# Performance work log

Measured on AMD Instinct MI355X. Metric: run time of the kernel, lower is better.

## Reference

```python
import jax, jax.numpy as jnp
import numpy as np

B, S, D = 4, 2048, 128


def setup_inputs() -> dict:
    key = jax.random.key(0)
    kq, kk, kv = jax.random.split(key, 3)
    query = jax.random.normal(kq, (B, S, D), dtype=jnp.float32)
    key_t = jax.random.normal(kk, (B, S, D), dtype=jnp.float32)
    value = jax.random.normal(kv, (B, S, D), dtype=jnp.float32)
    return {"query": query, "key": key_t, "value": value}


def reference(query, key, value):
    # Raw dot-general attention: contract only the last dim, NO batch dims,
    # so scores have shape [B, Sq, B, Sk] (cross-batch attention).
    scores = jnp.einsum('aqd,bkd->aqbk', query, key)  # [B,S,B,S]
    # softmax over the trailing half of the dims (axes 2 and 3 jointly)
    attn = jax.nn.softmax(scores, axis=(2, 3))
    # Dropout: train=False -> deterministic no-op.
    # Second dot_general contracts trailing (B,Sk) of attn with leading (B,Sk) of value.
    y = jnp.einsum('aqbk,bkd->aqd', attn, value)  # [B,S,D]
    return y
```

## Files before the change

### kernel.cpp

```cpp
#include <hip/hip_runtime.h>
#include <hip/hip_bf16.h>
#include <string.h>

#define NROWS 8192
#define DH    128
#define G     8
#define KPG   (NROWS / G)
#define NIT   (KPG / 64)
#define B32U  (16 * 512)
#define LOG2E 1.44269504088896340736f
#define MSCALED (56.0f * LOG2E)

typedef __attribute__((ext_vector_type(8)))  short    short8;
typedef __attribute__((ext_vector_type(16))) float    floatx16;
typedef __attribute__((ext_vector_type(4)))  unsigned short us4;
typedef __attribute__((ext_vector_type(8)))  _Float16 half8;
typedef __attribute__((ext_vector_type(4)))  _Float16 half4;

#define MFMA_BF32(a, b, c)  __builtin_amdgcn_mfma_f32_32x32x16_bf16((a), (b), (c), 0, 0, 0)
#define MFMA_F16W(a, b, c)  __builtin_amdgcn_mfma_f32_32x32x16_f16((a), (b), (c), 0, 0, 0)

__device__ __forceinline__ unsigned short f32_to_bf16(float f) {
    union { float f; unsigned u; } v; v.f = f;
    unsigned u = v.u + 0x7FFFu + ((v.u >> 16) & 1u);
    return (unsigned short)(u >> 16);
}
__device__ __forceinline__ float bf16_to_f32(unsigned short h) {
    union { unsigned u; float f; } v; v.u = ((unsigned)h) << 16;
    return v.f;
}
__device__ __forceinline__ float fast_exp2(float x) {
    float r; asm("v_exp_f32 %0, %1" : "=v"(r) : "v"(x)); return r;
}
__device__ __forceinline__ void async_ld16(const void* g, void* lds) {
    __builtin_amdgcn_global_load_lds(
        (const __attribute__((address_space(1))) unsigned int*)g,
        (__attribute__((address_space(3))) unsigned int*)lds, 16, 0, 0);
}

__global__ void prep_kernel(const float* __restrict__ Q, const float* __restrict__ K,
                            const float* __restrict__ V,
                            _Float16* __restrict__ Qf, unsigned short* __restrict__ KV) {
    int bid = blockIdx.x;
    if (bid < 1024) {
        int i = bid * 1024 + threadIdx.x * 4;
        float4 q = *(const float4*)(Q + i);
        half4 o = {(_Float16)q.x, (_Float16)q.y, (_Float16)q.z, (_Float16)q.w};
        *(half4*)(Qf + i) = o;
        return;
    }
    if (bid < 1152) {
        int B = bid - 1024;
        const float* Ksrc = K + (size_t)B * 64 * DH;
        unsigned short* dst = KV + (size_t)(2 * B) * B32U;
#pragma unroll
        for (int j = 0; j < 4; j++) {
            int ch = j * 256 + threadIdx.x;
            int mt = ch >> 9;
            int rem = ch & 511;
            int c = rem >> 6;
            int within = rem & 63;
            int h = within >> 5, l31 = within & 31;
            const float* src = Ksrc + (size_t)(mt * 32 + l31) * DH + c * 16 + h * 8;
            float4 a = *(const float4*)src;
            float4 b = *(const float4*)(src + 4);
            half8 o = {(_Float16)a.x, (_Float16)a.y, (_Float16)a.z, (_Float16)a.w,
                       (_Float16)b.x, (_Float16)b.y, (_Float16)b.z, (_Float16)b.w};
            *(half8*)(dst + (size_t)mt * B32U + c * 512 + within * 8) = o;
        }
        return;
    }
    int B = bid - 1152;
    __shared__ unsigned short tile[64][132];
    const float* Vsrc = V + (size_t)B * 64 * DH;
    {
        int row = threadIdx.x >> 2;
        int cb0 = (threadIdx.x & 3) * 32;
#pragma unroll
        for (int j = 0; j < 8; j++) {
            float4 v = *(const float4*)(Vsrc + (size_t)row * DH + cb0 + j * 4);
            tile[row][cb0 + j * 4 + 0] = f32_to_bf16(v.x);
            tile[row][cb0 + j * 4 + 1] = f32_to_bf16(v.y);
            tile[row][cb0 + j * 4 + 2] = f32_to_bf16(v.z);
            tile[row][cb0 + j * 4 + 3] = f32_to_bf16(v.w);
        }
    }
    __syncthreads();
    unsigned short* dstv = KV + (size_t)(2 * B) * B32U + 8 * 512;
#pragma unroll
    for (int j = 0; j < 4; j++) {
        int ch = j * 256 + threadIdx.x;
        int mt = ch >> 9;
        int rem = ch & 511;
        int seg = rem >> 6;
        int within = rem & 63;
        int h = within >> 5, rr = within & 31;
        int t = seg >> 1, sp = seg & 1;
        int d = t * 32 + rr;
        short8 o;
#pragma unroll
        for (int jj = 0; jj < 8; jj++) {
            int p = mt * 32 + sp * 16 + h * 8 + jj;
            int ar = (p & ~12) | ((p & 8) >> 1) | ((p & 4) << 1);
            o[jj] = tile[ar][d];
        }
        *(short8*)(dstv + (size_t)mt * B32U + seg * 512 + within * 8) = o;
    }
}

__launch_bounds__(256, 2)
__global__ void attn_kernel(const _Float16* __restrict__ Qf,
                            const unsigned short* __restrict__ KV,
                            unsigned short* __restrict__ Opart,
                            float* __restrict__ lsum) {
    __shared__ __align__(16) unsigned short kvbuf[2][32 * 512];

    const int lane = threadIdx.x & 63;
    const int wave = threadIdx.x >> 6;
    const int g    = blockIdx.x & (G - 1);
    const int qt   = blockIdx.x >> 3;
    const int l31  = lane & 31;
    const int h    = lane >> 5;
    const int qrow0 = qt * 128 + wave * 32;

    half8 qf[8];
    {
        const half8* ph = (const half8*)(Qf + (size_t)(qrow0 + l31) * DH + h * 8);
#pragma unroll
        for (int c = 0; c < 8; c++) qf[c] = ph[c * 2];
    }

    floatx16 Oacc[4];
#pragma unroll
    for (int t = 0; t < 4; t++)
#pragma unroll
        for (int e = 0; e < 16; e++) Oacc[t][e] = 0.f;
    float lacc = 0.f;

    const unsigned short* pb = KV + (size_t)(g * (KPG / 32)) * B32U + lane * 8;
    auto stage = [&](int buf) {
        unsigned short* dst = kvbuf[buf];
#pragma unroll
        for (int j = 0; j < 8; j++) {
            int s = wave + 4 * j;
            async_ld16(pb + s * 512, dst + s * 512);
        }
        pb += 2 * B32U;
    };

    const int fo = lane * 8;

    stage(0);
    for (int it = 0; it < NIT; ++it) {
        __syncthreads();
        if (it + 1 < NIT) stage((it + 1) & 1);

        const unsigned short* cb = kvbuf[it & 1];

        floatx16 S0, S1;
#pragma unroll
        for (int e = 0; e < 16; e++) { S0[e] = 0.f; S1[e] = 0.f; }
        __builtin_amdgcn_s_setprio(1);
#pragma unroll
        for (int c = 0; c < 8; c++) {
            half8 a0 = *(const half8*)(cb + c * 512 + fo);
            half8 a1 = *(const half8*)(cb + (16 + c) * 512 + fo);
            S0 = MFMA_F16W(a0, qf[c], S0);
            S1 = MFMA_F16W(a1, qf[c], S1);
        }
        __builtin_amdgcn_s_setprio(0);

        short8 bp0[2], bp1[2];
        auto expack = [&](const floatx16& S, short8 (&bp)[2]) {
#pragma unroll
            for (int sp = 0; sp < 2; sp++) {
                union { unsigned u[4]; short8 s8; } pk;
                float l0 = 0.f, l1 = 0.f;
#pragma unroll
                for (int e = 0; e < 4; e++) {
                    float pa  = fast_exp2(__builtin_fmaf(S[8 * sp + 2 * e],     LOG2E, -MSCALED));
                    float pb2 = fast_exp2(__builtin_fmaf(S[8 * sp + 2 * e + 1], LOG2E, -MSCALED));
                    l0 += pa; l1 += pb2;
                    __hip_bfloat162 c2 = __float22bfloat162_rn(float2{pa, pb2});
                    unsigned u; memcpy(&u, &c2, 4);
                    pk.u[e] = u;
                }
                lacc += l0 + l1;
                bp[sp] = pk.s8;
            }
        };
        expack(S0, bp0);
        expack(S1, bp1);

        __builtin_amdgcn_s_setprio(1);
#pragma unroll
        for (int sp = 0; sp < 2; sp++)
#pragma unroll
            for (int t = 0; t < 4; t++) {
                short8 vf0 = *(const short8*)(cb + (8 + t * 2 + sp) * 512 + fo);
                Oacc[t] = MFMA_BF32(vf0, bp0[sp], Oacc[t]);
                short8 vf1 = *(const short8*)(cb + (16 + 8 + t * 2 + sp) * 512 + fo);
                Oacc[t] = MFMA_BF32(vf1, bp1[sp], Oacc[t]);
            }
        __builtin_amdgcn_s_setprio(0);
    }

    unsigned short* op = Opart + ((size_t)g * NROWS + qrow0 + l31) * DH;
#pragma unroll
    for (int t = 0; t < 4; t++)
#pragma unroll
        for (int rg = 0; rg < 4; rg++) {
            us4 w;
#pragma unroll
            for (int e = 0; e < 4; e++) w[e] = f32_to_bf16(Oacc[t][4 * rg + e]);
            *(us4*)(op + 32 * t + 8 * rg + 4 * h) = w;
        }
    lacc += __shfl_xor(lacc, 32);
    if (h == 0) lsum[(size_t)g * NROWS + qrow0 + l31] = lacc;
}

__global__ void merge_kernel(const unsigned short* __restrict__ Opart,
                             const float* __restrict__ lsum, float* __restrict__ out) {
    int t = blockIdx.x * 256 + threadIdx.x;
    int base = t * 8;
    int q = base >> 7;
    float L = 0.f;
#pragma unroll
    for (int g = 0; g < G; g++) L += lsum[(size_t)g * NROWS + q];
    float acc[8] = {0.f, 0.f, 0.f, 0.f, 0.f, 0.f, 0.f, 0.f};
#pragma unroll
    for (int g = 0; g < G; g++) {
        short8 v = *(const short8*)(Opart + (size_t)g * NROWS * DH + base);
#pragma unroll
        for (int j = 0; j < 8; j++) acc[j] += bf16_to_f32((unsigned short)v[j]);
    }
    float inv = 1.0f / L;
    float4 o0 = {acc[0] * inv, acc[1] * inv, acc[2] * inv, acc[3] * inv};
    float4 o1 = {acc[4] * inv, acc[5] * inv, acc[6] * inv, acc[7] * inv};
    *(float4*)(out + base) = o0;
    *(float4*)(out + base + 4) = o1;
}

extern "C" void kernel_launch(void* const* d_in, const int* in_sizes, int n_in,
                              void* d_out, int out_size, void* d_ws, size_t ws_size,
                              hipStream_t stream) {
    const float* Q = (const float*)d_in[0];
    const float* K = (const float*)d_in[1];
    const float* V = (const float*)d_in[2];
    float* out = (float*)d_out;

    char* ws = (char*)d_ws;
    _Float16* Qf = (_Float16*)ws;
    unsigned short* KV = (unsigned short*)(ws + (size_t)NROWS * DH * 2);
    char* p = ws + (size_t)NROWS * DH * 2 + (size_t)(NROWS / 32) * B32U * 2;
    unsigned short* Opart = (unsigned short*)p;
    float* lsum = (float*)(p + (size_t)G * NROWS * DH * sizeof(unsigned short));

    hipLaunchKernelGGL(prep_kernel, dim3(1024 + 128 + 128), dim3(256), 0, stream,
                       Q, K, V, Qf, KV);
    hipLaunchKernelGGL(attn_kernel, dim3((NROWS / 128) * G), dim3(256), 0, stream,
                       Qf, KV, Opart, lsum);
    hipLaunchKernelGGL(merge_kernel, dim3(NROWS * DH / (256 * 8)), dim3(256), 0, stream,
                       Opart, lsum, out);
}
```

Baseline: 113.4 us.

## Fuse Q conversion into attention, widen blocks to 8 waves, split keys 16 ways

The separate Q fp32-to-fp16 conversion pass is dropped, and each attention wave now converts its own Q rows on load, which removes a kernel phase and a workspace round trip. Attention blocks grow to 512 threads covering 256 query rows, so each staged K/V tile in LDS is shared by twice as many waves. The key split G goes from 8 to 16. The inner loop now processes one 32-key sub-tile at a time, interleaving exp/pack with the PV MFMAs, which lowers register pressure to fit the new launch bounds. In exchange, the merge kernel reads twice as many partial outputs and there are fewer loop iterations per block.

```diff
diff --git a/kernel.cpp b/kernel.cpp
--- a/kernel.cpp
+++ b/kernel.cpp
@@ -4,7 +4,7 @@
 
 #define NROWS 8192
 #define DH    128
-#define G     8
+#define G     16
 #define KPG   (NROWS / G)
 #define NIT   (KPG / 64)
 #define B32U  (16 * 512)
@@ -15,7 +15,6 @@
 typedef __attribute__((ext_vector_type(16))) float    floatx16;
 typedef __attribute__((ext_vector_type(4)))  unsigned short us4;
 typedef __attribute__((ext_vector_type(8)))  _Float16 half8;
-typedef __attribute__((ext_vector_type(4)))  _Float16 half4;
 
 #define MFMA_BF32(a, b, c)  __builtin_amdgcn_mfma_f32_32x32x16_bf16((a), (b), (c), 0, 0, 0)
 #define MFMA_F16W(a, b, c)  __builtin_amdgcn_mfma_f32_32x32x16_f16((a), (b), (c), 0, 0, 0)
@@ -38,19 +37,11 @@
         (__attribute__((address_space(3))) unsigned int*)lds, 16, 0, 0);
 }
 
-__global__ void prep_kernel(const float* __restrict__ Q, const float* __restrict__ K,
-                            const float* __restrict__ V,
-                            _Float16* __restrict__ Qf, unsigned short* __restrict__ KV) {
+__global__ void prep_kernel(const float* __restrict__ K, const float* __restrict__ V,
+                            unsigned short* __restrict__ KV) {
     int bid = blockIdx.x;
-    if (bid < 1024) {
-        int i = bid * 1024 + threadIdx.x * 4;
-        float4 q = *(const float4*)(Q + i);
-        half4 o = {(_Float16)q.x, (_Float16)q.y, (_Float16)q.z, (_Float16)q.w};
-        *(half4*)(Qf + i) = o;
-        return;
-    }
-    if (bid < 1152) {
-        int B = bid - 1024;
+    if (bid < 128) {
+        int B = bid;
         const float* Ksrc = K + (size_t)B * 64 * DH;
         unsigned short* dst = KV + (size_t)(2 * B) * B32U;
 #pragma unroll
@@ -70,7 +61,7 @@
         }
         return;
     }
-    int B = bid - 1152;
+    int B = bid - 128;
     __shared__ unsigned short tile[64][132];
     const float* Vsrc = V + (size_t)B * 64 * DH;
     {
@@ -108,8 +99,8 @@
     }
 }
 
-__launch_bounds__(256, 2)
-__global__ void attn_kernel(const _Float16* __restrict__ Qf,
+__launch_bounds__(512, 4)
+__global__ void attn_kernel(const float* __restrict__ Q,
                             const unsigned short* __restrict__ KV,
                             unsigned short* __restrict__ Opart,
                             float* __restrict__ lsum) {
@@ -118,16 +109,21 @@
     const int lane = threadIdx.x & 63;
     const int wave = threadIdx.x >> 6;
     const int g    = blockIdx.x & (G - 1);
-    const int qt   = blockIdx.x >> 3;
+    const int qt   = blockIdx.x / G;
     const int l31  = lane & 31;
     const int h    = lane >> 5;
-    const int qrow0 = qt * 128 + wave * 32;
+    const int qrow0 = qt * 256 + wave * 32;
 
     half8 qf[8];
     {
-        const half8* ph = (const half8*)(Qf + (size_t)(qrow0 + l31) * DH + h * 8);
-#pragma unroll
-        for (int c = 0; c < 8; c++) qf[c] = ph[c * 2];
+        const float* qs = Q + (size_t)(qrow0 + l31) * DH + h * 8;
+#pragma unroll
+        for (int c = 0; c < 8; c++) {
+            float4 a = *(const float4*)(qs + c * 16);
+            float4 b = *(const float4*)(qs + c * 16 + 4);
+            qf[c] = half8{(_Float16)a.x, (_Float16)a.y, (_Float16)a.z, (_Float16)a.w,
+                          (_Float16)b.x, (_Float16)b.y, (_Float16)b.z, (_Float16)b.w};
+        }
     }
 
     floatx16 Oacc[4];
@@ -141,8 +137,8 @@
     auto stage = [&](int buf) {
         unsigned short* dst = kvbuf[buf];
 #pragma unroll
-        for (int j = 0; j < 8; j++) {
-            int s = wave + 4 * j;
+        for (int j = 0; j < 4; j++) {
+            int s = wave + 8 * j;
             async_ld16(pb + s * 512, dst + s * 512);
         }
         pb += 2 * B32U;
@@ -157,21 +153,21 @@
 
         const unsigned short* cb = kvbuf[it & 1];
 
-        floatx16 S0, S1;
-#pragma unroll
-        for (int e = 0; e < 16; e++) { S0[e] = 0.f; S1[e] = 0.f; }
-        __builtin_amdgcn_s_setprio(1);
-#pragma unroll
-        for (int c = 0; c < 8; c++) {
-            half8 a0 = *(const half8*)(cb + c * 512 + fo);
-            half8 a1 = *(const half8*)(cb + (16 + c) * 512 + fo);
-            S0 = MFMA_F16W(a0, qf[c], S0);
-            S1 = MFMA_F16W(a1, qf[c], S1);
-        }
-        __builtin_amdgcn_s_setprio(0);
-
-        short8 bp0[2], bp1[2];
-        auto expack = [&](const floatx16& S, short8 (&bp)[2]) {
+#pragma unroll
+        for (int mt = 0; mt < 2; mt++) {
+            const unsigned short* cm = cb + mt * B32U;
+
+            floatx16 S;
+#pragma unroll
+            for (int e = 0; e < 16; e++) S[e] = 0.f;
+            __builtin_amdgcn_s_setprio(1);
+#pragma unroll
+            for (int c = 0; c < 8; c++) {
+                half8 a = *(const half8*)(cm + c * 512 + fo);
+                S = MFMA_F16W(a, qf[c], S);
+            }
+            __builtin_amdgcn_s_setprio(0);
+
 #pragma unroll
             for (int sp = 0; sp < 2; sp++) {
                 union { unsigned u[4]; short8 s8; } pk;
@@ -186,23 +182,15 @@
                     pk.u[e] = u;
                 }
                 lacc += l0 + l1;
-                bp[sp] = pk.s8;
+                __builtin_amdgcn_s_setprio(1);
+#pragma unroll
+                for (int t = 0; t < 4; t++) {
+                    short8 vf = *(const short8*)(cm + (8 + t * 2 + sp) * 512 + fo);
+                    Oacc[t] = MFMA_BF32(vf, pk.s8, Oacc[t]);
+                }
+                __builtin_amdgcn_s_setprio(0);
             }
-        };
-        expack(S0, bp0);
-        expack(S1, bp1);
-
-        __builtin_amdgcn_s_setprio(1);
-#pragma unroll
-        for (int sp = 0; sp < 2; sp++)
-#pragma unroll
-            for (int t = 0; t < 4; t++) {
-                short8 vf0 = *(const short8*)(cb + (8 + t * 2 + sp) * 512 + fo);
-                Oacc[t] = MFMA_BF32(vf0, bp0[sp], Oacc[t]);
-                short8 vf1 = *(const short8*)(cb + (16 + 8 + t * 2 + sp) * 512 + fo);
-                Oacc[t] = MFMA_BF32(vf1, bp1[sp], Oacc[t]);
-            }
-        __builtin_amdgcn_s_setprio(0);
+        }
     }
 
     unsigned short* op = Opart + ((size_t)g * NROWS + qrow0 + l31) * DH;
@@ -250,16 +238,14 @@
     float* out = (float*)d_out;
 
     char* ws = (char*)d_ws;
-    _Float16* Qf = (_Float16*)ws;
-    unsigned short* KV = (unsigned short*)(ws + (size_t)NROWS * DH * 2);
-    char* p = ws + (size_t)NROWS * DH * 2 + (size_t)(NROWS / 32) * B32U * 2;
+    unsigned short* KV = (unsigned short*)ws;
+    char* p = ws + (size_t)(NROWS / 32) * B32U * 2;
     unsigned short* Opart = (unsigned short*)p;
     float* lsum = (float*)(p + (size_t)G * NROWS * DH * sizeof(unsigned short));
 
-    hipLaunchKernelGGL(prep_kernel, dim3(1024 + 128 + 128), dim3(256), 0, stream,
-                       Q, K, V, Qf, KV);
-    hipLaunchKernelGGL(attn_kernel, dim3((NROWS / 128) * G), dim3(256), 0, stream,
-                       Qf, KV, Opart, lsum);
+    hipLaunchKernelGGL(prep_kernel, dim3(256), dim3(256), 0, stream, K, V, KV);
+    hipLaunchKernelGGL(attn_kernel, dim3((NROWS / 256) * G), dim3(512), 0, stream,
+                       Q, KV, Opart, lsum);
     hipLaunchKernelGGL(merge_kernel, dim3(NROWS * DH / (256 * 8)), dim3(256), 0, stream,
                        Opart, lsum, out);
 }
```

Result: slower. 146.6 us (+29.3%).
